# Optimization experiments

Hardware: AMD Instinct MI355X
Metric: run time of the kernel (lower is better)

## Reference

```python
import jax, jax.numpy as jnp
import numpy as np

M = 8192          # tokens
DIM = 2048        # per-stream width; K = 4*DIM
S = 4             # fixed stream count (Stream4 kernels)
N = 32            # fixed GEMM output width
SINKHORN_ITERS = 20


def setup_inputs() -> dict:
    key = jax.random.key(0)
    k1, k2 = jax.random.split(key)
    X = jax.random.normal(k1, (M, S * DIM), dtype=jnp.float32)
    # scale W so H = X @ W is O(1): keeps sigmoid/exp/sinkhorn numerically sane
    W = jax.random.normal(k2, (S * DIM, N), dtype=jnp.float32) / np.float32(np.sqrt(S * DIM))
    # module init: beta = zeros(24), alpha = ones(3), concatenated
    alpha_beta = jnp.concatenate([jnp.zeros(24, jnp.float32), jnp.ones(3, jnp.float32)])
    return {"X": X, "W": W, "alpha_beta": alpha_beta}


def _sinkhorn(P, iters=SINKHORN_ITERS):
    # doubly-stochastic normalization of [M, S, S] matrices
    for _ in range(iters):
        P = P / jnp.sum(P, axis=-1, keepdims=True)  # row normalize
        P = P / jnp.sum(P, axis=-2, keepdims=True)  # col normalize
    return P


def reference(X, W, alpha_beta):
    Mm, K = X.shape
    d = K // S
    # skinny GEMM producing the mixing logits (fused w/ SplitK in the kernel)
    H = X @ W                                   # [M, 32]
    b_res, b_pre, b_pos = alpha_beta[0:16], alpha_beta[16:20], alpha_beta[20:24]
    a_res, a_pre, a_pos = alpha_beta[24], alpha_beta[25], alpha_beta[26]
    H_pre = a_pre * jax.nn.sigmoid(H[:, 16:20]) + b_pre          # [M, 4]
    H_pos = a_pos * jax.nn.sigmoid(H[:, 20:24]) + b_pos          # [M, 4]
    H_res = (a_res * H[:, 0:16] + b_res).reshape(Mm, S, S)       # [M, 4, 4]
    H_res = _sinkhorn(jnp.exp(H_res))                            # doubly stochastic
    # view X as 4 streams of width d
    Xs = X.reshape(Mm, S, d)                                     # [M, 4, d]
    # ApplyPreTransform: collapse streams with H_pre weights
    Y = jnp.einsum('ms,msd->md', H_pre, Xs)                      # [M, d]
    # ApplyResidual: per-token 4x4 stream mix + broadcast of pre-transformed feature
    O = jnp.einsum('msi,mid->msd', H_res, Xs) + H_pos[:, :, None] * Y[:, None, :]
    return O.reshape(Mm, K)
```

## Files before the change

kernel.cpp:

```cpp
#include <hip/hip_runtime.h>
#include <math.h>
#include <stdint.h>

#define K_DIM 8192
#define D_DIM 2048
#define M_ROWS 8192
#define N_W 32
#define NC 24
#define KSPLIT 32
#define KRANGE (K_DIM / KSPLIT)
#define KSB 8
#define RPB 128
#define THREADS 256

typedef short bf16x8 __attribute__((ext_vector_type(8)));
typedef float f32x4 __attribute__((ext_vector_type(4)));
union U32x4 { uint32_t u[4]; bf16x8 v; };

#define WFRAG_IDX(ks, tile, hilo) ((((ks) * 2 + (tile)) * 2 + (hilo)) * 64)

__global__ __launch_bounds__(256) void mhc_prepack_kernel(
    const float* __restrict__ W, unsigned short* __restrict__ wfrag,
    float* __restrict__ Hsum)
{
    const int idx = blockIdx.x * 256 + threadIdx.x;
    const int k = idx >> 5, n = idx & 31;
    const float w = W[(size_t)k * N_W + n];
    const uint32_t u = __float_as_uint(w);
    const float hif = __uint_as_float(u & 0xFFFF0000u);
    const uint32_t ur = __float_as_uint(w - hif);

    const int ks = k >> 5, kk = k & 31;
    const int lane = ((kk >> 3) << 4) | (n & 15);
    const int e = kk & 7;
    const int tile = n >> 4;
    unsigned short* p = wfrag + ((size_t)WFRAG_IDX(ks, tile, 0) + lane) * 8 + e;
    p[0]   = (unsigned short)(u >> 16);
    p[512] = (unsigned short)(ur >> 16);

    if (idx < M_ROWS * NC) Hsum[idx] = 0.f;
}

__global__ __launch_bounds__(THREADS, 4) void mhc_gemm_kernel(
    const float* __restrict__ X, const unsigned short* __restrict__ wfrag,
    float* __restrict__ Hsum)
{
    __shared__ __align__(16) unsigned short bfr[KSB][2][2][64][8];
    const int t = threadIdx.x;
    const int l = t & 63;
    const int wv = t >> 6;
    const int rowbase = blockIdx.x * RPB;
    const int kbase = blockIdx.y * KRANGE;

    {
        const float4* __restrict__ src = reinterpret_cast<const float4*>(
            wfrag + (size_t)blockIdx.y * (KSB * 2 * 2 * 64 * 8));
        float4* dst = reinterpret_cast<float4*>(&bfr[0][0][0][0][0]);
#pragma unroll
        for (int q = 0; q < 8; ++q)
            dst[q * THREADS + t] = src[q * THREADS + t];
    }
    __syncthreads();

#pragma unroll
    for (int tt = 0; tt < 2; ++tt) {
        const int tile16 = wv + tt * 4;
        const int arow = rowbase + tile16 * 16 + (l & 15);
        const float* __restrict__ xp =
            X + (size_t)arow * K_DIM + kbase + ((l >> 4) << 3);

        f32x4 c0 = {0.f, 0.f, 0.f, 0.f};
        f32x4 c1 = {0.f, 0.f, 0.f, 0.f};

#pragma unroll
        for (int s = 0; s < KSB; ++s) {
            const float4 xa = *reinterpret_cast<const float4*>(xp + s * 32);
            const float4 xb = *reinterpret_cast<const float4*>(xp + s * 32 + 4);
            float xs[8];
            xs[0] = xa.x; xs[1] = xa.y; xs[2] = xa.z; xs[3] = xa.w;
            xs[4] = xb.x; xs[5] = xb.y; xs[6] = xb.z; xs[7] = xb.w;

            U32x4 ah, al;
#pragma unroll
            for (int p = 0; p < 4; ++p) {
                const uint32_t u0 = __float_as_uint(xs[2 * p]);
                const uint32_t u1 = __float_as_uint(xs[2 * p + 1]);
                const float h0 = __uint_as_float(u0 & 0xFFFF0000u);
                const float h1 = __uint_as_float(u1 & 0xFFFF0000u);
                const uint32_t r0 = __float_as_uint(xs[2 * p] - h0);
                const uint32_t r1 = __float_as_uint(xs[2 * p + 1] - h1);
                ah.u[p] = (u1 & 0xFFFF0000u) | (u0 >> 16);
                al.u[p] = (r1 & 0xFFFF0000u) | (r0 >> 16);
            }

            const bf16x8 bh0 = *reinterpret_cast<const bf16x8*>(&bfr[s][0][0][l][0]);
            const bf16x8 bl0 = *reinterpret_cast<const bf16x8*>(&bfr[s][0][1][l][0]);
            const bf16x8 bh1 = *reinterpret_cast<const bf16x8*>(&bfr[s][1][0][l][0]);
            const bf16x8 bl1 = *reinterpret_cast<const bf16x8*>(&bfr[s][1][1][l][0]);

            c0 = __builtin_amdgcn_mfma_f32_16x16x32_bf16(ah.v, bh0, c0, 0, 0, 0);
            c0 = __builtin_amdgcn_mfma_f32_16x16x32_bf16(al.v, bh0, c0, 0, 0, 0);
            c0 = __builtin_amdgcn_mfma_f32_16x16x32_bf16(ah.v, bl0, c0, 0, 0, 0);
            c1 = __builtin_amdgcn_mfma_f32_16x16x32_bf16(ah.v, bh1, c1, 0, 0, 0);
            c1 = __builtin_amdgcn_mfma_f32_16x16x32_bf16(al.v, bh1, c1, 0, 0, 0);
            c1 = __builtin_amdgcn_mfma_f32_16x16x32_bf16(ah.v, bl1, c1, 0, 0, 0);
        }

        const int drow = rowbase + tile16 * 16 + ((l >> 4) << 2);
        const int col = l & 15;
#pragma unroll
        for (int r = 0; r < 4; ++r)
            atomicAdd(&Hsum[(size_t)(drow + r) * NC + col], c0[r]);
        if (col < 8) {
#pragma unroll
            for (int r = 0; r < 4; ++r)
                atomicAdd(&Hsum[(size_t)(drow + r) * NC + 16 + col], c1[r]);
        }
    }
}

__global__ __launch_bounds__(256) void mhc_apply_kernel(
    const float* __restrict__ X, const float* __restrict__ Hsum,
    const float* __restrict__ ab, float* __restrict__ out)
{
    __shared__ float pbuf[NC];
    const int row = blockIdx.x;
    const int t = threadIdx.x;

    if (t < 64) {
        const int lane = t;
        const float pl = (lane < NC) ? Hsum[(size_t)row * NC + lane] : 0.f;
        const float bias  = (lane < NC) ? ab[lane] : 0.f;
        const float scale = ab[(lane < 16) ? 24 : ((lane < 20) ? 25 : 26)];

        float vout;
        if (lane < 16) {
            vout = __expf(fmaf(scale, pl, bias));
        } else {
            vout = fmaf(scale, 1.f / (1.f + __expf(-pl)), bias);
        }

        float p = vout;
        for (int it = 0; it < 20; ++it) {
            float rs = p + __shfl_xor(p, 1);
            rs += __shfl_xor(rs, 2);
            p = p / rs;
            float cs = p + __shfl_xor(p, 4);
            cs += __shfl_xor(cs, 8);
            p = p / cs;
        }
        if (lane < NC) pbuf[lane] = (lane < 16) ? p : vout;
    }
    __syncthreads();

    float hres[4][4], hpre[4], hpos[4];
#pragma unroll
    for (int i = 0; i < 16; ++i) hres[i >> 2][i & 3] = pbuf[i];
#pragma unroll
    for (int i = 0; i < 4; ++i) hpre[i] = pbuf[16 + i];
#pragma unroll
    for (int i = 0; i < 4; ++i) hpos[i] = pbuf[20 + i];

    const float4* __restrict__ Xr =
        reinterpret_cast<const float4*>(X + (size_t)row * K_DIM);
    float4* __restrict__ Or = reinterpret_cast<float4*>(out + (size_t)row * K_DIM);

#pragma unroll
    for (int q = 0; q < 2; ++q) {
        const int pos = t + q * 256;
        float4 xq[4];
#pragma unroll
        for (int i = 0; i < 4; ++i) xq[i] = Xr[i * (D_DIM / 4) + pos];

        float y[4];
#pragma unroll
        for (int e = 0; e < 4; ++e) {
            float s = 0.f;
#pragma unroll
            for (int i = 0; i < 4; ++i)
                s = fmaf(hpre[i], reinterpret_cast<const float*>(&xq[i])[e], s);
            y[e] = s;
        }

#pragma unroll
        for (int s = 0; s < 4; ++s) {
            float4 o;
            float* oe = reinterpret_cast<float*>(&o);
#pragma unroll
            for (int e = 0; e < 4; ++e) {
                float v = hpos[s] * y[e];
#pragma unroll
                for (int i = 0; i < 4; ++i)
                    v = fmaf(hres[s][i], reinterpret_cast<const float*>(&xq[i])[e], v);
                oe[e] = v;
            }
            Or[s * (D_DIM / 4) + pos] = o;
        }
    }
}

extern "C" void kernel_launch(void* const* d_in, const int* in_sizes, int n_in,
                              void* d_out, int out_size, void* d_ws, size_t ws_size,
                              hipStream_t stream) {
    const float* X  = (const float*)d_in[0];
    const float* W  = (const float*)d_in[1];
    const float* ab = (const float*)d_in[2];
    float* out = (float*)d_out;
    unsigned short* wfrag = (unsigned short*)d_ws;
    float* Hsum = (float*)((char*)d_ws + 1048576);

    mhc_prepack_kernel<<<(K_DIM * N_W) / 256, 256, 0, stream>>>(W, wfrag, Hsum);
    dim3 g1(M_ROWS / RPB, KSPLIT);
    mhc_gemm_kernel<<<g1, THREADS, 0, stream>>>(X, wfrag, Hsum);
    mhc_apply_kernel<<<M_ROWS, 256, 0, stream>>>(X, Hsum, ab, out);
}
```

Measured before the change: 193.2 us.

## Stage X tiles through double-buffered LDS and cut split-K atomics

Restructures the split-K GEMM. It now uses fewer K splits (8 instead of 32) and 64 rows per block, so there are four times fewer atomicAdd partial-sum writes to Hsum. X is streamed in 64-wide K chunks through double-buffered, padded shared memory, with the next chunk's global load issued before the current chunk's MFMAs, to overlap memory latency with compute. W fragments are now read straight from global memory (L2-cached) rather than preloaded into LDS. The trade-off is fewer, longer-running blocks, which may reduce occupancy and latency hiding, plus an extra trip through LDS for X.

```diff
diff --git a/kernel.cpp b/kernel.cpp
--- a/kernel.cpp
+++ b/kernel.cpp
@@ -7,11 +7,13 @@
 #define M_ROWS 8192
 #define N_W 32
 #define NC 24
-#define KSPLIT 32
+#define KSPLIT 8
 #define KRANGE (K_DIM / KSPLIT)
-#define KSB 8
-#define RPB 128
+#define RPB 64
 #define THREADS 256
+#define CHUNKK 64
+#define NCHUNK (KRANGE / CHUNKK)
+#define PADF 68
 
 typedef short bf16x8 __attribute__((ext_vector_type(8)));
 typedef float f32x4 __attribute__((ext_vector_type(4)));
@@ -45,37 +47,50 @@
     const float* __restrict__ X, const unsigned short* __restrict__ wfrag,
     float* __restrict__ Hsum)
 {
-    __shared__ __align__(16) unsigned short bfr[KSB][2][2][64][8];
+    __shared__ __align__(16) float Xl[2][RPB * PADF];
     const int t = threadIdx.x;
     const int l = t & 63;
     const int wv = t >> 6;
     const int rowbase = blockIdx.x * RPB;
     const int kbase = blockIdx.y * KRANGE;
 
-    {
-        const float4* __restrict__ src = reinterpret_cast<const float4*>(
-            wfrag + (size_t)blockIdx.y * (KSB * 2 * 2 * 64 * 8));
-        float4* dst = reinterpret_cast<float4*>(&bfr[0][0][0][0][0]);
-#pragma unroll
-        for (int q = 0; q < 8; ++q)
-            dst[q * THREADS + t] = src[q * THREADS + t];
-    }
+    f32x4 c0 = {0.f, 0.f, 0.f, 0.f};
+    f32x4 c1 = {0.f, 0.f, 0.f, 0.f};
+    const float4* __restrict__ Xg = reinterpret_cast<const float4*>(X);
+    const bf16x8* __restrict__ wf = reinterpret_cast<const bf16x8*>(wfrag);
+
+    float4 pf[4];
+    auto LOADREGS = [&](int c) {
+#pragma unroll
+        for (int q = 0; q < 4; ++q) {
+            const int F = q * THREADS + t;
+            const int row = F >> 4, slot = F & 15;
+            pf[q] = Xg[(size_t)(rowbase + row) * (K_DIM / 4)
+                       + ((kbase + c * CHUNKK) >> 2) + slot];
+        }
+    };
+    auto WRITELDS = [&](int b) {
+#pragma unroll
+        for (int q = 0; q < 4; ++q) {
+            const int F = q * THREADS + t;
+            const int row = F >> 4, slot = F & 15;
+            *reinterpret_cast<float4*>(&Xl[b][row * PADF + slot * 4]) = pf[q];
+        }
+    };
+
+    LOADREGS(0);
+    WRITELDS(0);
     __syncthreads();
 
-#pragma unroll
-    for (int tt = 0; tt < 2; ++tt) {
-        const int tile16 = wv + tt * 4;
-        const int arow = rowbase + tile16 * 16 + (l & 15);
-        const float* __restrict__ xp =
-            X + (size_t)arow * K_DIM + kbase + ((l >> 4) << 3);
-
-        f32x4 c0 = {0.f, 0.f, 0.f, 0.f};
-        f32x4 c1 = {0.f, 0.f, 0.f, 0.f};
-
-#pragma unroll
-        for (int s = 0; s < KSB; ++s) {
-            const float4 xa = *reinterpret_cast<const float4*>(xp + s * 32);
-            const float4 xb = *reinterpret_cast<const float4*>(xp + s * 32 + 4);
+    for (int c = 0; c < NCHUNK; ++c) {
+        if (c + 1 < NCHUNK) LOADREGS(c + 1);
+
+        const float* xt = &Xl[c & 1][(wv * 16 + (l & 15)) * PADF + ((l >> 4) << 3)];
+#pragma unroll
+        for (int ksl = 0; ksl < 2; ++ksl) {
+            const int ks = blockIdx.y * (KRANGE / 32) + c * 2 + ksl;
+            const float4 xa = *reinterpret_cast<const float4*>(xt + ksl * 32);
+            const float4 xb = *reinterpret_cast<const float4*>(xt + ksl * 32 + 4);
             float xs[8];
             xs[0] = xa.x; xs[1] = xa.y; xs[2] = xa.z; xs[3] = xa.w;
             xs[4] = xb.x; xs[5] = xb.y; xs[6] = xb.z; xs[7] = xb.w;
@@ -93,10 +108,10 @@
                 al.u[p] = (r1 & 0xFFFF0000u) | (r0 >> 16);
             }
 
-            const bf16x8 bh0 = *reinterpret_cast<const bf16x8*>(&bfr[s][0][0][l][0]);
-            const bf16x8 bl0 = *reinterpret_cast<const bf16x8*>(&bfr[s][0][1][l][0]);
-            const bf16x8 bh1 = *reinterpret_cast<const bf16x8*>(&bfr[s][1][0][l][0]);
-            const bf16x8 bl1 = *reinterpret_cast<const bf16x8*>(&bfr[s][1][1][l][0]);
+            const bf16x8 bh0 = wf[WFRAG_IDX(ks, 0, 0) + l];
+            const bf16x8 bl0 = wf[WFRAG_IDX(ks, 0, 1) + l];
+            const bf16x8 bh1 = wf[WFRAG_IDX(ks, 1, 0) + l];
+            const bf16x8 bl1 = wf[WFRAG_IDX(ks, 1, 1) + l];
 
             c0 = __builtin_amdgcn_mfma_f32_16x16x32_bf16(ah.v, bh0, c0, 0, 0, 0);
             c0 = __builtin_amdgcn_mfma_f32_16x16x32_bf16(al.v, bh0, c0, 0, 0, 0);
@@ -106,16 +121,21 @@
             c1 = __builtin_amdgcn_mfma_f32_16x16x32_bf16(ah.v, bl1, c1, 0, 0, 0);
         }
 
-        const int drow = rowbase + tile16 * 16 + ((l >> 4) << 2);
-        const int col = l & 15;
+        if (c + 1 < NCHUNK) {
+            WRITELDS((c + 1) & 1);
+            __syncthreads();
+        }
+    }
+
+    const int drow = rowbase + wv * 16 + ((l >> 4) << 2);
+    const int col = l & 15;
+#pragma unroll
+    for (int r = 0; r < 4; ++r)
+        atomicAdd(&Hsum[(size_t)(drow + r) * NC + col], c0[r]);
+    if (col < 8) {
 #pragma unroll
         for (int r = 0; r < 4; ++r)
-            atomicAdd(&Hsum[(size_t)(drow + r) * NC + col], c0[r]);
-        if (col < 8) {
-#pragma unroll
-            for (int r = 0; r < 4; ++r)
-                atomicAdd(&Hsum[(size_t)(drow + r) * NC + 16 + col], c1[r]);
-        }
+            atomicAdd(&Hsum[(size_t)(drow + r) * NC + 16 + col], c1[r]);
     }
 }
 
```

Result: slower. 218.5 us (+13.1%).

## Restructure split-K GEMM with LDS-staged X tiles, in-block reduction, single-bf16 W

Applied to the files above, without the earlier changes.

The GEMM kernel now stages a 16-row by 512-column X tile in padded shared memory with coalesced float4 loads. Eight waves each take a different K slice of that tile, and their partial results are reduced in shared memory before one atomicAdd per output, which cuts global atomic traffic. W is now stored as a single rounded bf16 value instead of a hi/lo pair, so each step issues two MFMAs per tile instead of three. This lowers accuracy on the W side of the GEMM and changes the grid to many small blocks with 512 threads.

```diff
diff --git a/kernel.cpp b/kernel.cpp
--- a/kernel.cpp
+++ b/kernel.cpp
@@ -7,17 +7,18 @@
 #define M_ROWS 8192
 #define N_W 32
 #define NC 24
-#define KSPLIT 32
-#define KRANGE (K_DIM / KSPLIT)
-#define KSB 8
-#define RPB 128
-#define THREADS 256
+#define KSPLIT 16
+#define KRANGE 512
+#define KSB 16
+#define RPB 16
+#define THR 512
+#define PADF 516
 
 typedef short bf16x8 __attribute__((ext_vector_type(8)));
 typedef float f32x4 __attribute__((ext_vector_type(4)));
 union U32x4 { uint32_t u[4]; bf16x8 v; };
 
-#define WFRAG_IDX(ks, tile, hilo) ((((ks) * 2 + (tile)) * 2 + (hilo)) * 64)
+#define WFRAG_IDX(ks, tile) (((ks) * 2 + (tile)) * 64)
 
 __global__ __launch_bounds__(256) void mhc_prepack_kernel(
     const float* __restrict__ W, unsigned short* __restrict__ wfrag,
@@ -27,95 +28,106 @@
     const int k = idx >> 5, n = idx & 31;
     const float w = W[(size_t)k * N_W + n];
     const uint32_t u = __float_as_uint(w);
-    const float hif = __uint_as_float(u & 0xFFFF0000u);
-    const uint32_t ur = __float_as_uint(w - hif);
+    const uint32_t r = u + 0x7FFFu + ((u >> 16) & 1u);
 
     const int ks = k >> 5, kk = k & 31;
     const int lane = ((kk >> 3) << 4) | (n & 15);
     const int e = kk & 7;
     const int tile = n >> 4;
-    unsigned short* p = wfrag + ((size_t)WFRAG_IDX(ks, tile, 0) + lane) * 8 + e;
-    p[0]   = (unsigned short)(u >> 16);
-    p[512] = (unsigned short)(ur >> 16);
+    wfrag[((size_t)WFRAG_IDX(ks, tile) + lane) * 8 + e] = (unsigned short)(r >> 16);
 
     if (idx < M_ROWS * NC) Hsum[idx] = 0.f;
 }
 
-__global__ __launch_bounds__(THREADS, 4) void mhc_gemm_kernel(
+__global__ __launch_bounds__(THR, 4) void mhc_gemm_kernel(
     const float* __restrict__ X, const unsigned short* __restrict__ wfrag,
     float* __restrict__ Hsum)
 {
-    __shared__ __align__(16) unsigned short bfr[KSB][2][2][64][8];
+    __shared__ __align__(16) float Xl[RPB * PADF];
+    __shared__ __align__(16) unsigned short bfr[KSB * 2 * 64 * 8];
+    __shared__ float Hpart[8][RPB][NC];
+
     const int t = threadIdx.x;
     const int l = t & 63;
     const int wv = t >> 6;
     const int rowbase = blockIdx.x * RPB;
-    const int kbase = blockIdx.y * KRANGE;
+    const int kb4 = blockIdx.y * (KRANGE / 4);
+
+    const float4* __restrict__ Xg = reinterpret_cast<const float4*>(X);
+
+    float4 pf[4];
+#pragma unroll
+    for (int j = 0; j < 4; ++j)
+        pf[j] = Xg[(size_t)(rowbase + wv * 2 + (j >> 1)) * (K_DIM / 4)
+                   + kb4 + (j & 1) * 64 + l];
 
     {
-        const float4* __restrict__ src = reinterpret_cast<const float4*>(
-            wfrag + (size_t)blockIdx.y * (KSB * 2 * 2 * 64 * 8));
-        float4* dst = reinterpret_cast<float4*>(&bfr[0][0][0][0][0]);
-#pragma unroll
-        for (int q = 0; q < 8; ++q)
-            dst[q * THREADS + t] = src[q * THREADS + t];
-    }
+        const float4* __restrict__ bsrc = reinterpret_cast<const float4*>(
+            wfrag + (size_t)blockIdx.y * (KSB * 2 * 64 * 8));
+        float4* bdst = reinterpret_cast<float4*>(bfr);
+#pragma unroll
+        for (int i = 0; i < 4; ++i)
+            bdst[i * THR + t] = bsrc[i * THR + t];
+    }
+
+#pragma unroll
+    for (int j = 0; j < 4; ++j)
+        *reinterpret_cast<float4*>(
+            &Xl[(wv * 2 + (j >> 1)) * PADF + ((j & 1) * 64 + l) * 4]) = pf[j];
     __syncthreads();
 
-#pragma unroll
-    for (int tt = 0; tt < 2; ++tt) {
-        const int tile16 = wv + tt * 4;
-        const int arow = rowbase + tile16 * 16 + (l & 15);
-        const float* __restrict__ xp =
-            X + (size_t)arow * K_DIM + kbase + ((l >> 4) << 3);
-
-        f32x4 c0 = {0.f, 0.f, 0.f, 0.f};
-        f32x4 c1 = {0.f, 0.f, 0.f, 0.f};
-
-#pragma unroll
-        for (int s = 0; s < KSB; ++s) {
-            const float4 xa = *reinterpret_cast<const float4*>(xp + s * 32);
-            const float4 xb = *reinterpret_cast<const float4*>(xp + s * 32 + 4);
-            float xs[8];
-            xs[0] = xa.x; xs[1] = xa.y; xs[2] = xa.z; xs[3] = xa.w;
-            xs[4] = xb.x; xs[5] = xb.y; xs[6] = xb.z; xs[7] = xb.w;
-
-            U32x4 ah, al;
-#pragma unroll
-            for (int p = 0; p < 4; ++p) {
-                const uint32_t u0 = __float_as_uint(xs[2 * p]);
-                const uint32_t u1 = __float_as_uint(xs[2 * p + 1]);
-                const float h0 = __uint_as_float(u0 & 0xFFFF0000u);
-                const float h1 = __uint_as_float(u1 & 0xFFFF0000u);
-                const uint32_t r0 = __float_as_uint(xs[2 * p] - h0);
-                const uint32_t r1 = __float_as_uint(xs[2 * p + 1] - h1);
-                ah.u[p] = (u1 & 0xFFFF0000u) | (u0 >> 16);
-                al.u[p] = (r1 & 0xFFFF0000u) | (r0 >> 16);
-            }
-
-            const bf16x8 bh0 = *reinterpret_cast<const bf16x8*>(&bfr[s][0][0][l][0]);
-            const bf16x8 bl0 = *reinterpret_cast<const bf16x8*>(&bfr[s][0][1][l][0]);
-            const bf16x8 bh1 = *reinterpret_cast<const bf16x8*>(&bfr[s][1][0][l][0]);
-            const bf16x8 bl1 = *reinterpret_cast<const bf16x8*>(&bfr[s][1][1][l][0]);
-
-            c0 = __builtin_amdgcn_mfma_f32_16x16x32_bf16(ah.v, bh0, c0, 0, 0, 0);
-            c0 = __builtin_amdgcn_mfma_f32_16x16x32_bf16(al.v, bh0, c0, 0, 0, 0);
-            c0 = __builtin_amdgcn_mfma_f32_16x16x32_bf16(ah.v, bl0, c0, 0, 0, 0);
-            c1 = __builtin_amdgcn_mfma_f32_16x16x32_bf16(ah.v, bh1, c1, 0, 0, 0);
-            c1 = __builtin_amdgcn_mfma_f32_16x16x32_bf16(al.v, bh1, c1, 0, 0, 0);
-            c1 = __builtin_amdgcn_mfma_f32_16x16x32_bf16(ah.v, bl1, c1, 0, 0, 0);
-        }
-
-        const int drow = rowbase + tile16 * 16 + ((l >> 4) << 2);
-        const int col = l & 15;
+    f32x4 c0 = {0.f, 0.f, 0.f, 0.f};
+    f32x4 c1 = {0.f, 0.f, 0.f, 0.f};
+    const bf16x8* __restrict__ bf = reinterpret_cast<const bf16x8*>(bfr);
+    const float* xbase = &Xl[(l & 15) * PADF + ((l >> 4) << 3)];
+
+#pragma unroll
+    for (int u = 0; u < 2; ++u) {
+        const int ksl = wv * 2 + u;
+        const float4 xa = *reinterpret_cast<const float4*>(xbase + ksl * 32);
+        const float4 xb = *reinterpret_cast<const float4*>(xbase + ksl * 32 + 4);
+        float xs[8];
+        xs[0] = xa.x; xs[1] = xa.y; xs[2] = xa.z; xs[3] = xa.w;
+        xs[4] = xb.x; xs[5] = xb.y; xs[6] = xb.z; xs[7] = xb.w;
+
+        U32x4 ah, al;
+#pragma unroll
+        for (int p = 0; p < 4; ++p) {
+            const uint32_t u0 = __float_as_uint(xs[2 * p]);
+            const uint32_t u1 = __float_as_uint(xs[2 * p + 1]);
+            const float h0 = __uint_as_float(u0 & 0xFFFF0000u);
+            const float h1 = __uint_as_float(u1 & 0xFFFF0000u);
+            const uint32_t r0 = __float_as_uint(xs[2 * p] - h0);
+            const uint32_t r1 = __float_as_uint(xs[2 * p + 1] - h1);
+            ah.u[p] = (u1 & 0xFFFF0000u) | (u0 >> 16);
+            al.u[p] = (r1 & 0xFFFF0000u) | (r0 >> 16);
+        }
+
+        const bf16x8 bh0 = bf[WFRAG_IDX(ksl, 0) + l];
+        const bf16x8 bh1 = bf[WFRAG_IDX(ksl, 1) + l];
+
+        c0 = __builtin_amdgcn_mfma_f32_16x16x32_bf16(ah.v, bh0, c0, 0, 0, 0);
+        c0 = __builtin_amdgcn_mfma_f32_16x16x32_bf16(al.v, bh0, c0, 0, 0, 0);
+        c1 = __builtin_amdgcn_mfma_f32_16x16x32_bf16(ah.v, bh1, c1, 0, 0, 0);
+        c1 = __builtin_amdgcn_mfma_f32_16x16x32_bf16(al.v, bh1, c1, 0, 0, 0);
+    }
+
+#pragma unroll
+    for (int r = 0; r < 4; ++r)
+        Hpart[wv][((l >> 4) << 2) + r][l & 15] = c0[r];
+    if ((l & 15) < 8) {
 #pragma unroll
         for (int r = 0; r < 4; ++r)
-            atomicAdd(&Hsum[(size_t)(drow + r) * NC + col], c0[r]);
-        if (col < 8) {
-#pragma unroll
-            for (int r = 0; r < 4; ++r)
-                atomicAdd(&Hsum[(size_t)(drow + r) * NC + 16 + col], c1[r]);
-        }
+            Hpart[wv][((l >> 4) << 2) + r][16 + (l & 15)] = c1[r];
+    }
+    __syncthreads();
+
+    if (t < RPB * NC) {
+        const int row = t / NC, col = t % NC;
+        float h = 0.f;
+#pragma unroll
+        for (int w = 0; w < 8; ++w) h += Hpart[w][row][col];
+        atomicAdd(&Hsum[(size_t)(rowbase + row) * NC + col], h);
     }
 }
 
@@ -207,10 +219,10 @@
     const float* ab = (const float*)d_in[2];
     float* out = (float*)d_out;
     unsigned short* wfrag = (unsigned short*)d_ws;
-    float* Hsum = (float*)((char*)d_ws + 1048576);
+    float* Hsum = (float*)((char*)d_ws + 524288);
 
     mhc_prepack_kernel<<<(K_DIM * N_W) / 256, 256, 0, stream>>>(W, wfrag, Hsum);
     dim3 g1(M_ROWS / RPB, KSPLIT);
-    mhc_gemm_kernel<<<g1, THREADS, 0, stream>>>(X, wfrag, Hsum);
+    mhc_gemm_kernel<<<g1, THR, 0, stream>>>(X, wfrag, Hsum);
     mhc_apply_kernel<<<M_ROWS, 256, 0, stream>>>(X, Hsum, ab, out);
 }
```

Result: faster. 172.3 us (-10.9%).
